# Optimization experiments

Hardware: AMD Instinct MI355X
Metric: run time of the kernel (lower is better)

The kernel has to match this reference:

```python
import jax, jax.numpy as jnp
import numpy as np

N, D, NUM_CLASSES = 4096, 512, 128
MARGIN = 0.3


def setup_inputs() -> dict:
    key = jax.random.key(0)
    k1, k2 = jax.random.split(key)
    embeddings = jax.random.normal(k1, (N, D), dtype=jnp.float32)
    labels = jax.random.randint(k2, (N,), 0, NUM_CLASSES, dtype=jnp.int64)
    return {"embeddings": embeddings, "labels": labels}


def _batch_hard_triplet(embeddings, labels, margin):
    # L2-normalize rows (torch F.normalize: x / max(||x||, eps))
    norm = jnp.linalg.norm(embeddings, axis=1, keepdims=True)
    e = embeddings / jnp.maximum(norm, 1e-12)
    n = e.shape[0]
    # Pairwise Euclidean distance via Gram matrix; ||a-b||^2 = 2 - 2 a.b for unit vectors
    gram = e @ e.T                                   # [N, N]
    sq = jnp.clip(2.0 - 2.0 * gram, 0.0, None)
    # safe sqrt: zero (and exactly-equal) pairs get distance 0 with zero gradient
    nz = sq > 0
    dist = jnp.where(nz, jnp.sqrt(jnp.where(nz, sq, 1.0)), 0.0)  # [N, N]

    same = labels[:, None] == labels[None, :]        # [N, N] bool
    eye = jnp.eye(n, dtype=bool)
    pos_mask = same & ~eye                           # positives excluding self
    neg_mask = ~same

    # hardest positive (row max over positives), hardest negative (row min over negatives)
    dist_ap = jnp.max(jnp.where(pos_mask, dist, -jnp.inf), axis=1)  # [N]
    dist_an = jnp.min(jnp.where(neg_mask, dist, jnp.inf), axis=1)   # [N]

    valid = jnp.any(pos_mask, axis=1) & jnp.any(neg_mask, axis=1)   # rows kept by torch loop
    per_row = jax.nn.relu(dist_ap - dist_an + margin)
    num_valid = jnp.sum(valid)
    loss_sum = jnp.sum(jnp.where(valid, per_row, 0.0))
    return jnp.where(num_valid > 0, loss_sum / jnp.maximum(num_valid, 1), 0.0)


def reference(embeddings, labels):
    return _batch_hard_triplet(embeddings, labels, MARGIN)
```

## Files before the change

### kernel.cpp

```cpp
#include <hip/hip_runtime.h>
#include <hip/hip_bf16.h>
#include <stdint.h>


#define NROW 4096
#define DIM  512
#define MARGIN 0.3f
#define BT 128
#define NTILE (NROW / BT)
#define NPAIR (NTILE * (NTILE + 1) / 2)
#define POS_INIT 0xFFFFFFFFu
#define NEG_INIT 0u

typedef __attribute__((ext_vector_type(8))) __bf16 bf16x8;
typedef __attribute__((ext_vector_type(4))) float  f32x4;
typedef __attribute__((ext_vector_type(8))) unsigned short u16x8;

__device__ __forceinline__ unsigned enc(float f) {
    unsigned u = __float_as_uint(f);
    return (u & 0x80000000u) ? ~u : (u | 0x80000000u);
}
__device__ __forceinline__ float dec(unsigned e) {
    return (e & 0x80000000u) ? __uint_as_float(e & 0x7fffffffu)
                             : __uint_as_float(~e);
}

__device__ __forceinline__ unsigned short f2bf(float f) {
    __hip_bfloat16 h = __float2bfloat16(f);
    return *reinterpret_cast<unsigned short*>(&h);
}

__global__ void tl_norm(const float* __restrict__ E,
                        __hip_bfloat16* __restrict__ Ebf,
                        unsigned* __restrict__ posArr,
                        unsigned* __restrict__ negArr) {
    if (blockIdx.x < 16) {
        int t = blockIdx.x * 256 + threadIdx.x;
        posArr[t] = POS_INIT;
        negArr[t] = NEG_INIT;
    }
    const int wave  = threadIdx.x >> 6;
    const int lane  = threadIdx.x & 63;
    const int r2    = lane >> 4;
    const int kc    = lane & 15;
    const int rtile = blockIdx.x;
    const int r_in  = wave * 4 + r2;
    const int row   = rtile * 16 + r_in;

    const float4* src = (const float4*)(E + (size_t)row * DIM) + kc * 8;
    float4 v[8];
    #pragma unroll
    for (int i = 0; i < 8; i++) v[i] = src[i];

    float ss = 0.0f;
    #pragma unroll
    for (int i = 0; i < 8; i++)
        ss += v[i].x*v[i].x + v[i].y*v[i].y + v[i].z*v[i].z + v[i].w*v[i].w;
    #pragma unroll
    for (int m = 1; m < 16; m <<= 1) ss += __shfl_xor(ss, m);
    const float inv = 1.0f / fmaxf(sqrtf(ss), 1e-12f);

    u16x8* dst = (u16x8*)Ebf + (size_t)kc * 16384 + (size_t)rtile * 64 + r_in;
    #pragma unroll
    for (int c = 0; c < 4; c++) {
        const float4 lo = v[2*c], hi = v[2*c + 1];
        u16x8 o;
        o[0] = f2bf(lo.x * inv); o[1] = f2bf(lo.y * inv);
        o[2] = f2bf(lo.z * inv); o[3] = f2bf(lo.w * inv);
        o[4] = f2bf(hi.x * inv); o[5] = f2bf(hi.y * inv);
        o[6] = f2bf(hi.z * inv); o[7] = f2bf(hi.w * inv);
        dst[c * 16] = o;
    }
}

__global__ void __launch_bounds__(256, 2)
tl_gram(const __hip_bfloat16* __restrict__ Ebf,
        const int* __restrict__ labels,
        unsigned* __restrict__ posArr,
        unsigned* __restrict__ negArr) {
    __shared__ int rowLab[BT];
    __shared__ int colLab[BT];

    const int bid = blockIdx.x;
    int t = (bid & 7) * (NPAIR / 8) + (bid >> 3);

    int bi = 0, rowlen = NTILE;
    while (t >= rowlen) { t -= rowlen; rowlen--; bi++; }
    const int bj = bi + t;

    const int tid  = threadIdx.x;
    const int wave = tid >> 6;
    const int lane = tid & 63;
    const int quad = lane >> 4;
    const int l16  = lane & 15;
    const int wr   = wave >> 1;
    const int wc   = wave & 1;
    const int tileI = bi * BT;
    const int tileJ = bj * BT;
    const bool diag = (bi == bj);

    if (tid < BT) rowLab[tid] = labels[tileI + tid];
    else          colLab[tid - BT] = labels[tileJ + (tid - BT)];
    __syncthreads();

    const bf16x8* Ev = (const bf16x8*)Ebf;
    const bf16x8* Ea = Ev + ((tileI + wr * 64) >> 4) * 64 + lane;
    const bf16x8* Eb = Ev + ((tileJ + wc * 64) >> 4) * 64 + lane;

    f32x4 acc[4][4] = {};
    bf16x8 a[4][4], b[4][4];

    #pragma unroll
    for (int p = 0; p < 3; ++p) {
        #pragma unroll
        for (int i = 0; i < 4; i++) {
            a[p][i] = Ea[p * 16384 + i * 64];
            b[p][i] = Eb[p * 16384 + i * 64];
        }
    }
    __builtin_amdgcn_sched_barrier(0);

    #pragma unroll
    for (int kk = 0; kk < 16; ++kk) {
        const int cur = kk & 3;
        if (kk + 3 < 16) {
            const int nx = (kk + 3) & 3;
            #pragma unroll
            for (int i = 0; i < 4; i++) {
                a[nx][i] = Ea[(kk + 3) * 16384 + i * 64];
                b[nx][i] = Eb[(kk + 3) * 16384 + i * 64];
            }
        }
        __builtin_amdgcn_sched_barrier(0);
        #pragma unroll
        for (int mi = 0; mi < 4; mi++)
            #pragma unroll
            for (int ni = 0; ni < 4; ni++)
                acc[mi][ni] = __builtin_amdgcn_mfma_f32_16x16x32_bf16(
                    a[cur][mi], b[cur][ni], acc[mi][ni], 0, 0, 0);
        __builtin_amdgcn_sched_barrier(0);
    }

    int rl[16], cl[4], clocv[4];
    #pragma unroll
    for (int mi = 0; mi < 4; mi++)
        #pragma unroll
        for (int reg = 0; reg < 4; reg++)
            rl[mi * 4 + reg] = rowLab[wr * 64 + mi * 16 + quad * 4 + reg];
    #pragma unroll
    for (int ni = 0; ni < 4; ni++) {
        clocv[ni] = wc * 64 + ni * 16 + l16;
        cl[ni] = colLab[clocv[ni]];
    }

    #pragma unroll
    for (int mi = 0; mi < 4; mi++) {
        #pragma unroll
        for (int reg = 0; reg < 4; reg++) {
            const int rloc = wr * 64 + mi * 16 + quad * 4 + reg;
            const int lr   = rl[mi * 4 + reg];
            const int gi   = tileI + rloc;
            float pmin =  INFINITY;
            float nmax = -INFINITY;
            #pragma unroll
            for (int ni = 0; ni < 4; ni++) {
                const int gj  = tileJ + clocv[ni];
                const float g = acc[mi][ni][reg];
                const bool same = (lr == cl[ni]);
                if (same && gi != gj) pmin = fminf(pmin, g);
                if (!same)            nmax = fmaxf(nmax, g);
            }
            #pragma unroll
            for (int m = 1; m < 16; m <<= 1) {
                pmin = fminf(pmin, __shfl_xor(pmin, m));
                nmax = fmaxf(nmax, __shfl_xor(nmax, m));
            }
            if (l16 == 0) {
                if (pmin <  INFINITY) atomicMin(&posArr[gi], enc(pmin));
                if (nmax > -INFINITY) atomicMax(&negArr[gi], enc(nmax));
            }
        }
    }

    if (!diag) {
        #pragma unroll
        for (int ni = 0; ni < 4; ni++) {
            const int lc = cl[ni];
            const int gj = tileJ + clocv[ni];
            float pmin =  INFINITY;
            float nmax = -INFINITY;
            #pragma unroll
            for (int mi = 0; mi < 4; mi++) {
                #pragma unroll
                for (int reg = 0; reg < 4; reg++) {
                    const float g = acc[mi][ni][reg];
                    const bool same = (rl[mi * 4 + reg] == lc);
                    if (same) pmin = fminf(pmin, g);
                    else      nmax = fmaxf(nmax, g);
                }
            }
            pmin = fminf(pmin, __shfl_xor(pmin, 16));
            pmin = fminf(pmin, __shfl_xor(pmin, 32));
            nmax = fmaxf(nmax, __shfl_xor(nmax, 16));
            nmax = fmaxf(nmax, __shfl_xor(nmax, 32));
            if (quad == 0) {
                if (pmin <  INFINITY) atomicMin(&posArr[gj], enc(pmin));
                if (nmax > -INFINITY) atomicMax(&negArr[gj], enc(nmax));
            }
        }
    }
}

__global__ void tl_final(const unsigned* __restrict__ posArr,
                         const unsigned* __restrict__ negArr,
                         float* __restrict__ out) {
    const int tid = threadIdx.x;
    uint4 pe4 = ((const uint4*)posArr)[tid];
    uint4 ne4 = ((const uint4*)negArr)[tid];
    unsigned pes[4] = {pe4.x, pe4.y, pe4.z, pe4.w};
    unsigned nes[4] = {ne4.x, ne4.y, ne4.z, ne4.w};
    float sum = 0.0f;
    int   count = 0;
    #pragma unroll
    for (int j = 0; j < 4; j++) {
        const bool valid = (pes[j] != POS_INIT) && (nes[j] != NEG_INIT);
        const float dap = sqrtf(fmaxf(2.0f - 2.0f * dec(pes[j]), 0.0f));
        const float dan = sqrtf(fmaxf(2.0f - 2.0f * dec(nes[j]), 0.0f));
        const float per = fmaxf(dap - dan + MARGIN, 0.0f);
        if (valid) { sum += per; count += 1; }
    }
    #pragma unroll
    for (int m = 32; m >= 1; m >>= 1) {
        sum   += __shfl_xor(sum, m);
        count += __shfl_xor(count, m);
    }
    __shared__ float ssum[16];
    __shared__ int   scnt[16];
    const int wave = tid >> 6, lane = tid & 63;
    if (lane == 0) { ssum[wave] = sum; scnt[wave] = count; }
    __syncthreads();
    if (tid == 0) {
        float s = 0.0f; int c = 0;
        #pragma unroll
        for (int w = 0; w < 16; w++) { s += ssum[w]; c += scnt[w]; }
        out[0] = (c > 0) ? (s / (float)c) : 0.0f;
    }
}

extern "C" void kernel_launch(void* const* d_in, const int* in_sizes, int n_in,
                              void* d_out, int out_size, void* d_ws, size_t ws_size,
                              hipStream_t stream) {
    const float* E      = (const float*)d_in[0];
    const int*   labels = (const int*)d_in[1];
    float*       out    = (float*)d_out;

    char* ws = (char*)d_ws;
    __hip_bfloat16* Ebf   = (__hip_bfloat16*)ws;
    unsigned* posArr      = (unsigned*)(ws + (size_t)NROW * DIM * 2);
    unsigned* negArr      = posArr + NROW;

    tl_norm<<<NROW / 16, 256, 0, stream>>>(E, Ebf, posArr, negArr);
    tl_gram<<<NPAIR, 256, 0, stream>>>(Ebf, labels, posArr, negArr);
    tl_final<<<1, 1024, 0, stream>>>(posArr, negArr, out);
}
```

Measured before the change: 92.60 us.

## Stage Gram tiles through LDS with async global-to-LDS double buffering

Each wave used to load its A and B fragments straight from global memory into registers with a 4-deep prefetch, so every A row-tile was fetched by two waves and every B tile by two waves. Now the block copies each k-slab of the A and B tiles into double-buffered shared memory using the global_load_lds builtin, and all waves read their fragments from LDS. This halves redundant global/L2 traffic and frees registers, at the cost of 64KB of LDS, a __syncthreads per stage, and extra LDS reads. The larger LDS footprint may limit how many blocks fit per CU.

Result: slower. 98.06 us (+5.9%).

```diff
diff --git a/kernel.cpp b/kernel.cpp
--- a/kernel.cpp
+++ b/kernel.cpp
@@ -30,6 +30,13 @@
     return *reinterpret_cast<unsigned short*>(&h);
 }
 
+__device__ __forceinline__ void async_copy16(const void* g, void* l) {
+    __builtin_amdgcn_global_load_lds(
+        (const __attribute__((address_space(1))) unsigned int*)g,
+        (__attribute__((address_space(3))) unsigned int*)l,
+        16, 0, 0);
+}
+
 __global__ void tl_norm(const float* __restrict__ E,
                         __hip_bfloat16* __restrict__ Ebf,
                         unsigned* __restrict__ posArr,
@@ -78,6 +85,7 @@
         const int* __restrict__ labels,
         unsigned* __restrict__ posArr,
         unsigned* __restrict__ negArr) {
+    __shared__ uint4 ldsAB[2][32][64];
     __shared__ int rowLab[BT];
     __shared__ int colLab[BT];
 
@@ -101,44 +109,52 @@
 
     if (tid < BT) rowLab[tid] = labels[tileI + tid];
     else          colLab[tid - BT] = labels[tileJ + (tid - BT)];
+
+    const int rtI0 = tileI >> 4;
+    const int rtJ0 = tileJ >> 4;
+    const uint4* Ev = (const uint4*)Ebf;
+
+    auto stage = [&](int nbuf, int s) {
+        const int kkBase = 2 * s;
+        #pragma unroll
+        for (int q = 0; q < 8; ++q) {
+            const int ca  = wave * 8 + q;
+            const int cc  = ca & 15;
+            const int kl  = cc >> 3;
+            const int rt  = cc & 7;
+            const int rt0 = (ca >= 16) ? rtJ0 : rtI0;
+            const uint4* src = Ev + (size_t)(kkBase + kl) * 16384
+                                  + (size_t)(rt0 + rt) * 64 + lane;
+            async_copy16(src, &ldsAB[nbuf][ca][0]);
+        }
+    };
+
+    f32x4 acc[4][4] = {};
+
+    stage(0, 0);
     __syncthreads();
 
-    const bf16x8* Ev = (const bf16x8*)Ebf;
-    const bf16x8* Ea = Ev + ((tileI + wr * 64) >> 4) * 64 + lane;
-    const bf16x8* Eb = Ev + ((tileJ + wc * 64) >> 4) * 64 + lane;
-
-    f32x4 acc[4][4] = {};
-    bf16x8 a[4][4], b[4][4];
-
-    #pragma unroll
-    for (int p = 0; p < 3; ++p) {
-        #pragma unroll
-        for (int i = 0; i < 4; i++) {
-            a[p][i] = Ea[p * 16384 + i * 64];
-            b[p][i] = Eb[p * 16384 + i * 64];
-        }
-    }
-    __builtin_amdgcn_sched_barrier(0);
-
-    #pragma unroll
-    for (int kk = 0; kk < 16; ++kk) {
-        const int cur = kk & 3;
-        if (kk + 3 < 16) {
-            const int nx = (kk + 3) & 3;
-            #pragma unroll
-            for (int i = 0; i < 4; i++) {
-                a[nx][i] = Ea[(kk + 3) * 16384 + i * 64];
-                b[nx][i] = Eb[(kk + 3) * 16384 + i * 64];
-            }
-        }
-        __builtin_amdgcn_sched_barrier(0);
-        #pragma unroll
-        for (int mi = 0; mi < 4; mi++)
+    #pragma unroll
+    for (int s = 0; s < 8; ++s) {
+        const int cur = s & 1;
+        if (s < 7) stage(cur ^ 1, s + 1);
+        #pragma unroll
+        for (int kl = 0; kl < 2; ++kl) {
+            bf16x8 af[4], bg[4];
+            #pragma unroll
+            for (int mi = 0; mi < 4; mi++)
+                af[mi] = *(const bf16x8*)&ldsAB[cur][kl * 8 + wr * 4 + mi][lane];
             #pragma unroll
             for (int ni = 0; ni < 4; ni++)
-                acc[mi][ni] = __builtin_amdgcn_mfma_f32_16x16x32_bf16(
-                    a[cur][mi], b[cur][ni], acc[mi][ni], 0, 0, 0);
-        __builtin_amdgcn_sched_barrier(0);
+                bg[ni] = *(const bf16x8*)&ldsAB[cur][16 + kl * 8 + wc * 4 + ni][lane];
+            #pragma unroll
+            for (int mi = 0; mi < 4; mi++)
+                #pragma unroll
+                for (int ni = 0; ni < 4; ni++)
+                    acc[mi][ni] = __builtin_amdgcn_mfma_f32_16x16x32_bf16(
+                        af[mi], bg[ni], acc[mi][ni], 0, 0, 0);
+        }
+        __syncthreads();
     }
 
     int rl[16], cl[4], clocv[4];
```
